# Kernel tuning notes

Hardware: AMD Instinct MI355X
Metric: run time of the kernel (lower is better)

## Reference

```python
import jax, jax.numpy as jnp
import numpy as np

B, N, DIM = 2, 2048, 1024
HEADS, DH = 16, 64
INNER = HEADS * DH
LN_EPS = 1e-5


def setup_inputs() -> dict:
    key = jax.random.key(0)
    ks = jax.random.split(key, 3)
    x = jax.random.normal(ks[0], (B, N, DIM), dtype=jnp.float32)
    ln_w = jnp.ones((DIM,), dtype=jnp.float32)
    ln_b = jnp.zeros((DIM,), dtype=jnp.float32)
    w_qkv = jax.random.normal(ks[1], (DIM, 3 * INNER), dtype=jnp.float32) * (DIM ** -0.5)
    w_out = jax.random.normal(ks[2], (INNER, DIM), dtype=jnp.float32) * (INNER ** -0.5)
    b_out = jnp.zeros((DIM,), dtype=jnp.float32)
    return {"x": x, "ln_w": ln_w, "ln_b": ln_b, "w_qkv": w_qkv, "w_out": w_out, "b_out": b_out}


def _rope(q, k):
    # q, k: (b, h, n, d) with d even; interleaved RoPE matching the torch module.
    n, d = q.shape[-2], q.shape[-1]
    inv_freq = jnp.exp(jnp.arange(0, d, 2, dtype=jnp.float32) * (-jnp.log(jnp.float32(10000.0)) / d))
    ang = jnp.arange(n, dtype=jnp.float32)[:, None] * inv_freq[None, :]  # (n, d/2)
    cos = jnp.repeat(jnp.cos(ang), 2, axis=-1)  # (n, d) -> broadcast over b,h
    sin = jnp.repeat(jnp.sin(ang), 2, axis=-1)

    def rot(t):
        t2 = t.reshape(*t.shape[:-1], d // 2, 2)  # pairs (even, odd)
        t2 = jnp.stack([-t2[..., 1], t2[..., 0]], axis=-1).reshape(t.shape)
        return t * cos + t2 * sin

    return rot(q), rot(k)


def reference(x, ln_w, ln_b, w_qkv, w_out, b_out):
    # LayerNorm
    mu = jnp.mean(x, axis=-1, keepdims=True)
    var = jnp.var(x, axis=-1, keepdims=True)
    xn = (x - mu) * jax.lax.rsqrt(var + LN_EPS) * ln_w + ln_b
    # QKV projection (no bias)
    qkv = xn @ w_qkv  # (b, n, 3*inner)
    q, k, v = jnp.split(qkv, 3, axis=-1)
    split_heads = lambda t: t.reshape(B, N, HEADS, DH).transpose(0, 2, 1, 3)  # b h n d
    q, k, v = split_heads(q), split_heads(k), split_heads(v)
    q, k = _rope(q, k)
    scale = DH ** -0.5
    dots = jnp.einsum('bhid,bhjd->bhij', q, k) * scale
    attn = jax.nn.softmax(dots, axis=-1)
    out = jnp.einsum('bhij,bhjd->bhid', attn, v)
    out = out.transpose(0, 2, 1, 3).reshape(B, N, INNER)  # b n (h d)
    return out @ w_out + b_out
```

## Files before the change

### kernel.cpp

```cpp
#include <hip/hip_runtime.h>

typedef unsigned short u16;
typedef unsigned int   u32;
typedef __bf16 bf16x8 __attribute__((ext_vector_type(8)));
typedef __bf16 bf16x2 __attribute__((ext_vector_type(2)));
typedef float  f32x4  __attribute__((ext_vector_type(4)));

#define B_     2
#define N_     2048
#define DIM_   1024
#define HEADS_ 16
#define DH_    64
#define BH_    (B_*HEADS_)
#define ROWS_  (B_*N_)

__device__ __forceinline__ u16 f2b(float f) {
  union { __bf16 h; u16 u; } v; v.h = (__bf16)f; return v.u;
}
__device__ __forceinline__ u32 pkb(float a, float b) {
  bf16x2 t; t[0] = (__bf16)a; t[1] = (__bf16)b;
  union { bf16x2 v; u32 u; } c; c.v = t; return c.u;
}
__device__ __forceinline__ float b2f(u16 h) {
  union { u32 u; float f; } v; v.u = ((u32)h) << 16;
  return v.f;
}
__device__ __forceinline__ void gload16(const void* g, void* l) {
  __builtin_amdgcn_global_load_lds(
      (const __attribute__((address_space(1))) void*)g,
      (__attribute__((address_space(3))) void*)l, 16, 0, 0);
}
__device__ __forceinline__ f32x4 mfma16(bf16x8 a, bf16x8 b, f32x4 c) {
  return __builtin_amdgcn_mfma_f32_16x16x32_bf16(a, b, c, 0, 0, 0);
}

__global__ __launch_bounds__(256) void prep_kernel(
    const float* __restrict__ x, const float* __restrict__ lw,
    const float* __restrict__ lb, const float* __restrict__ wqkv,
    const float* __restrict__ wout, u16* __restrict__ xn,
    u16* __restrict__ wqt, u16* __restrict__ wot) {
  __shared__ float tile[32][33];
  int blk = blockIdx.x, t = threadIdx.x;
  if (blk < 4096) {
    int r = blk;
    const float4* xr = (const float4*)(x + (size_t)r * DIM_);
    float4 v = xr[t];
    float s  = v.x + v.y + v.z + v.w;
    float s2 = v.x*v.x + v.y*v.y + v.z*v.z + v.w*v.w;
    #pragma unroll
    for (int off = 32; off >= 1; off >>= 1) {
      s  += __shfl_down(s, off);
      s2 += __shfl_down(s2, off);
    }
    int w = t >> 6, lane = t & 63;
    if (lane == 0) { tile[0][w] = s; tile[1][w] = s2; }
    __syncthreads();
    if (t == 0) {
      float S = tile[0][0]+tile[0][1]+tile[0][2]+tile[0][3];
      float S2 = tile[1][0]+tile[1][1]+tile[1][2]+tile[1][3];
      float mu = S * (1.0f/DIM_);
      float var = S2 * (1.0f/DIM_) - mu*mu;
      tile[2][0] = mu; tile[2][1] = rsqrtf(var + 1e-5f);
    }
    __syncthreads();
    float mu = tile[2][0], rs = tile[2][1];
    float4 wv = ((const float4*)lw)[t];
    float4 bv = ((const float4*)lb)[t];
    u32 lo = pkb((v.x-mu)*rs*wv.x + bv.x, (v.y-mu)*rs*wv.y + bv.y);
    u32 hi = pkb((v.z-mu)*rs*wv.z + bv.z, (v.w-mu)*rs*wv.w + bv.w);
    ((uint2*)xn)[(size_t)r*256 + t] = make_uint2(lo, hi);
  } else {
    const float* in; u16* outp; int R, C, c0, r0;
    if (blk < 7168) {
      int b2 = blk - 4096;
      in = wqkv; outp = wqt; R = 1024; C = 3072;
      c0 = (b2 % 96) * 32; r0 = (b2 / 96) * 32;
    } else {
      int b2 = blk - 7168;
      in = wout; outp = wot; R = 1024; C = 1024;
      c0 = (b2 & 31) * 32; r0 = (b2 >> 5) * 32;
    }
    int tx = t & 31, ty = t >> 5;
    #pragma unroll
    for (int i = 0; i < 4; i++)
      tile[ty + i*8][tx] = in[(size_t)(r0 + ty + i*8) * C + c0 + tx];
    __syncthreads();
    #pragma unroll
    for (int i = 0; i < 4; i++)
      outp[(size_t)(c0 + ty + i*8) * R + r0 + tx] = f2b(tile[tx][ty + i*8]);
  }
}

__global__ __launch_bounds__(256) void gemm_qkv(
    const u16* __restrict__ A, const u16* __restrict__ Bt,
    u16* __restrict__ qo, u16* __restrict__ ko, u16* __restrict__ vo) {
  const int K = 1024;
  __shared__ __align__(16) u16 lA[128*32];
  __shared__ __align__(16) u16 lB[128*32];
  int tid = threadIdx.x;
  int lane = tid & 63;
  int w = tid >> 6, wm = w >> 1, wn = w & 1;
  int l15 = lane & 15, g = lane >> 4;
  int bm = blockIdx.x, bn = blockIdx.y;
  const f32x4 z = {0.f, 0.f, 0.f, 0.f};
  f32x4 acc[4][4];
  #pragma unroll
  for (int i = 0; i < 4; i++)
    #pragma unroll
    for (int j = 0; j < 4; j++)
      acc[i][j] = z;
  int sslot = (tid & 3) ^ ((tid >> 3) & 3);
  const u16* ag = A  + (size_t)(bm*128 + (tid>>2)) * K + sslot*8;
  const u16* bg = Bt + (size_t)(bn*128 + (tid>>2)) * K + sslot*8;
  u16* la = lA + tid*8;
  u16* lb = lB + tid*8;
  for (int k0 = 0; k0 < K; k0 += 32) {
    gload16(ag + k0,                la);
    gload16(ag + (size_t)64*K + k0, la + 2048);
    gload16(bg + k0,                lb);
    gload16(bg + (size_t)64*K + k0, lb + 2048);
    __syncthreads();
    bf16x8 af[4], bfr[4];
    #pragma unroll
    for (int mt = 0; mt < 4; mt++) {
      int R = wm*64 + mt*16 + l15;
      af[mt] = *(const bf16x8*)(lA + R*32 + (g ^ ((R >> 1) & 3))*8);
    }
    #pragma unroll
    for (int nt = 0; nt < 4; nt++) {
      int R = wn*64 + nt*16 + l15;
      bfr[nt] = *(const bf16x8*)(lB + R*32 + (g ^ ((R >> 1) & 3))*8);
    }
    __builtin_amdgcn_s_setprio(1);
    #pragma unroll
    for (int mt = 0; mt < 4; mt++)
      #pragma unroll
      for (int nt = 0; nt < 4; nt++)
        acc[mt][nt] = mfma16(af[mt], bfr[nt], acc[mt][nt]);
    __builtin_amdgcn_s_setprio(0);
    __syncthreads();
  }
  #pragma unroll
  for (int mt = 0; mt < 4; mt++) {
    #pragma unroll
    for (int nt = 0; nt < 4; nt++) {
      #pragma unroll
      for (int reg = 0; reg < 4; reg++) {
        int rr = bm*128 + wm*64 + mt*16 + g*4 + reg;
        int cc = bn*128 + wn*64 + nt*16 + l15;
        float val = acc[mt][nt][reg];
        int which = cc >> 10, inner = cc & 1023;
        int h = inner >> 6, dd = inner & 63;
        int b = rr >> 11, np = rr & 2047;
        int bh = b*HEADS_ + h;
        if (which == 0)      qo[((size_t)(bh*2048 + np))*64 + dd] = f2b(val);
        else if (which == 1) ko[((size_t)(bh*2048 + np))*64 + dd] = f2b(val);
        else                 vo[((size_t)(bh*64 + dd))*2048 + np] = f2b(val);
      }
    }
  }
}

__global__ __launch_bounds__(256) void rope_k_kernel(u16* k) {
  int tid = blockIdx.x * 256 + threadIdx.x;
  int row = tid >> 3, sub = tid & 7;
  int n = row & 2047;
  u32* kp = (u32*)(k + (size_t)row * 64 + sub * 8);
  uint4 uk = *(uint4*)kp;
  float c4[4], s4[4];
  #pragma unroll
  for (int j = 0; j < 4; j++) {
    int p = sub*4 + j;
    float freq = expf(-(2.0f * (float)p) * (9.210340371976184f / 64.0f));
    float ang = (float)n * freq;
    __sincosf(ang, &s4[j], &c4[j]);
  }
#define ROPE_K(u, c, s) { \
    float e = b2f((u16)(u)), o = b2f((u16)((u) >> 16)); \
    (u) = pkb(e*(c) - o*(s), o*(c) + e*(s)); }
  ROPE_K(uk.x, c4[0], s4[0]) ROPE_K(uk.y, c4[1], s4[1])
  ROPE_K(uk.z, c4[2], s4[2]) ROPE_K(uk.w, c4[3], s4[3])
#undef ROPE_K
  *(uint4*)kp = uk;
}

__global__ __launch_bounds__(256) void gemm_out(
    const u16* __restrict__ A, const u16* __restrict__ Bt,
    const float* __restrict__ bias, float* __restrict__ out) {
  const int K = 1024, N = 1024;
  __shared__ __align__(16) u16 lA[128*32];
  __shared__ __align__(16) u16 lB[64*32];
  int tid = threadIdx.x;
  int lane = tid & 63;
  int w = tid >> 6, wm = w >> 1, wn = w & 1;
  int l15 = lane & 15, g = lane >> 4;
  int bm = blockIdx.x, bn = blockIdx.y;
  const f32x4 z = {0.f, 0.f, 0.f, 0.f};
  f32x4 acc[4][2];
  #pragma unroll
  for (int i = 0; i < 4; i++)
    #pragma unroll
    for (int j = 0; j < 2; j++)
      acc[i][j] = z;
  int sslot = (tid & 3) ^ ((tid >> 3) & 3);
  const u16* ag = A  + (size_t)(bm*128 + (tid>>2)) * K + sslot*8;
  const u16* bg = Bt + (size_t)(bn*64 + (tid>>2)) * K + sslot*8;
  u16* la = lA + tid*8;
  u16* lb = lB + tid*8;
  for (int k0 = 0; k0 < K; k0 += 32) {
    gload16(ag + k0,                la);
    gload16(ag + (size_t)64*K + k0, la + 2048);
    gload16(bg + k0,                lb);
    __syncthreads();
    bf16x8 af[4], bfr[2];
    #pragma unroll
    for (int mt = 0; mt < 4; mt++) {
      int R = wm*64 + mt*16 + l15;
      af[mt] = *(const bf16x8*)(lA + R*32 + (g ^ ((R >> 1) & 3))*8);
    }
    #pragma unroll
    for (int nt = 0; nt < 2; nt++) {
      int R = wn*32 + nt*16 + l15;
      bfr[nt] = *(const bf16x8*)(lB + R*32 + (g ^ ((R >> 1) & 3))*8);
    }
    __builtin_amdgcn_s_setprio(1);
    #pragma unroll
    for (int mt = 0; mt < 4; mt++)
      #pragma unroll
      for (int nt = 0; nt < 2; nt++)
        acc[mt][nt] = mfma16(af[mt], bfr[nt], acc[mt][nt]);
    __builtin_amdgcn_s_setprio(0);
    __syncthreads();
  }
  #pragma unroll
  for (int mt = 0; mt < 4; mt++)
    #pragma unroll
    for (int nt = 0; nt < 2; nt++)
      #pragma unroll
      for (int reg = 0; reg < 4; reg++) {
        int rr = bm*128 + wm*64 + mt*16 + g*4 + reg;
        int cc = bn*64 + wn*32 + nt*16 + l15;
        out[(size_t)rr * N + cc] = acc[mt][nt][reg] + bias[cc];
      }
}

__global__ __launch_bounds__(512, 4) void flash_attn(
    const u16* __restrict__ qbf, const u16* __restrict__ kbf,
    const u16* __restrict__ vt, u16* __restrict__ aout) {
  __shared__ __align__(16) char smem[49152];
  int tid = threadIdx.x;
  int w = tid >> 6, lane = tid & 63;
  int l15 = lane & 15, g = lane >> 4;
  int p = w & 3, rho = w >> 2;
  int lin = blockIdx.x;
  int nb = (lin & 7) * 64 + (lin >> 3);
  int bh = nb >> 4, qb = nb & 15;
  const f32x4 z = {0.f, 0.f, 0.f, 0.f};
  const u16* qrow_base = qbf + ((size_t)bh*2048 + qb*128 + p*32) * 64;
  const float qs = 0.125f * 1.4426950408889634f;
  bf16x8 Qf[2][2];
  #pragma unroll
  for (int qt = 0; qt < 2; qt++) {
    int n = qb*128 + p*32 + qt*16 + l15;
    #pragma unroll
    for (int dh = 0; dh < 2; dh++) {
      union { bf16x8 v; u32 u[4]; } f;
      f.v = *(const bf16x8*)(qrow_base + (qt*16 + l15)*64 + dh*32 + g*8);
      #pragma unroll
      for (int j = 0; j < 4; j++) {
        int pidx = dh*16 + g*4 + j;
        float freq = expf(-(2.0f * (float)pidx) * (9.210340371976184f / 64.0f));
        float sn, cn;
        __sincosf((float)n * freq, &sn, &cn);
        float e = b2f((u16)f.u[j]), o = b2f((u16)(f.u[j] >> 16));
        f.u[j] = pkb((e*cn - o*sn)*qs, (o*cn + e*sn)*qs);
      }
      Qf[qt][dh] = f.v;
    }
  }
  const char* kb = (const char*)(kbf + (size_t)bh * 2048 * 64);
  const char* vb = (const char*)(vt  + (size_t)bh * 64 * 2048);
  int srow = tid >> 3;
  int soff = ((tid & 7) * 16) ^ ((srow & 7) << 4);
  int sl = srow & 31;
  int ksrc = (srow & 32) | (((sl >> 2) & 3) << 3) | (((sl >> 4) & 1) << 2) | (sl & 3);
  const int swz = (l15 & 7) << 4;

  const size_t kgo = (size_t)ksrc * 128 + soff;
  const size_t vgo = (size_t)srow * 4096 + soff;
  const int ldk = tid * 16;
  const int ldv = 24576 + tid * 16;
  int koff[2][2], voff[4];
  #pragma unroll
  for (int kt = 0; kt < 2; kt++)
    #pragma unroll
    for (int dh = 0; dh < 2; dh++)
      koff[kt][dh] = (rho*32 + kt*16 + l15)*128 + ((dh*64 + g*16) ^ swz);
  #pragma unroll
  for (int dt = 0; dt < 4; dt++)
    voff[dt] = 24576 + (dt*16 + l15)*128 + ((rho*64 + g*16) ^ swz);

  bf16x8 ones;
  #pragma unroll
  for (int i = 0; i < 8; i++) ones[i] = (__bf16)1.0f;

  f32x4 den[2] = {z, z};
  f32x4 o[4][2];
  #pragma unroll
  for (int i = 0; i < 4; i++)
    #pragma unroll
    for (int j = 0; j < 2; j++)
      o[i][j] = z;

#define STAGE(T, BUF) { \
    gload16(kb + (size_t)(T)*8192 + kgo, smem + (BUF)*8192 + ldk); \
    gload16(vb + (size_t)(T)*128  + vgo, smem + (BUF)*8192 + ldv); }

#define FBODY(T, CUR, PFB, DOSTAGE, WM) { \
    if (DOSTAGE) STAGE((T) + 2, PFB) \
    f32x4 st[2][2]; \
    bf16x8 ka[2][2]; \
    _Pragma("unroll") \
    for (int kt = 0; kt < 2; kt++) \
      _Pragma("unroll") \
      for (int dh = 0; dh < 2; dh++) \
        ka[kt][dh] = *(const bf16x8*)(smem + (CUR)*8192 + koff[kt][dh]); \
    __builtin_amdgcn_s_setprio(1); \
    _Pragma("unroll") \
    for (int kt = 0; kt < 2; kt++) \
      _Pragma("unroll") \
      for (int qt = 0; qt < 2; qt++) { \
        f32x4 a = mfma16(ka[kt][0], Qf[qt][0], z); \
        st[kt][qt] = mfma16(ka[kt][1], Qf[qt][1], a); \
      } \
    __builtin_amdgcn_s_setprio(0); \
    _Pragma("unroll") \
    for (int kt = 0; kt < 2; kt++) \
      _Pragma("unroll") \
      for (int qt = 0; qt < 2; qt++) \
        _Pragma("unroll") \
        for (int r = 0; r < 4; r++) \
          st[kt][qt][r] = __builtin_amdgcn_exp2f(st[kt][qt][r]); \
    bf16x8 vf[4]; \
    _Pragma("unroll") \
    for (int dt = 0; dt < 4; dt++) \
      vf[dt] = *(const bf16x8*)(smem + (CUR)*8192 + voff[dt]); \
    __builtin_amdgcn_s_setprio(1); \
    _Pragma("unroll") \
    for (int qt = 0; qt < 2; qt++) { \
      union { u32 u[4]; bf16x8 v; } pf; \
      pf.u[0] = pkb(st[0][qt][0], st[0][qt][1]); \
      pf.u[1] = pkb(st[0][qt][2], st[0][qt][3]); \
      pf.u[2] = pkb(st[1][qt][0], st[1][qt][1]); \
      pf.u[3] = pkb(st[1][qt][2], st[1][qt][3]); \
      den[qt] = mfma16(ones, pf.v, den[qt]); \
      _Pragma("unroll") \
      for (int dt = 0; dt < 4; dt++) \
        o[dt][qt] = mfma16(vf[dt], pf.v, o[dt][qt]); \
    } \
    __builtin_amdgcn_s_setprio(0); \
    if ((WM) == 2) { \
      asm volatile("s_waitcnt vmcnt(2)" ::: "memory"); \
      __builtin_amdgcn_s_barrier(); \
    } else if ((WM) == 0) { \
      asm volatile("s_waitcnt vmcnt(0)" ::: "memory"); \
      __builtin_amdgcn_s_barrier(); \
    } }

  STAGE(0, 0)
  STAGE(1, 1)
  asm volatile("s_waitcnt vmcnt(2)" ::: "memory");
  __builtin_amdgcn_s_barrier();

  #pragma unroll 1
  for (int tb = 0; tb < 30; tb += 3) {
    FBODY(tb + 0, 0, 2, 1, 2)
    FBODY(tb + 1, 1, 0, 1, 2)
    FBODY(tb + 2, 2, 1, 1, 2)
  }
  FBODY(30, 0, 0, 0, 0)
  FBODY(31, 1, 0, 0, 3)
#undef STAGE
#undef FBODY

  float ls[2] = {den[0][0], den[1][0]};
  __syncthreads();

  float* lspx = (float*)(smem + 32768);
  if (rho == 1) {
    #pragma unroll
    for (int dt = 0; dt < 4; dt++)
      #pragma unroll
      for (int qt = 0; qt < 2; qt++) {
        int ql = qt*16 + l15;
        int off = p*8192 + ql*256 + ((dt*64 + g*16) ^ ((ql & 7) << 4));
        *(f32x4*)(smem + off) = o[dt][qt];
      }
    if (g == 0) {
      lspx[p*64 + l15]      = ls[0];
      lspx[p*64 + 16 + l15] = ls[1];
    }
  }
  __syncthreads();
  float rls[2] = {0.f, 0.f};
  if (rho == 0) {
    #pragma unroll
    for (int qt = 0; qt < 2; qt++)
      rls[qt] = 1.0f / (ls[qt] + lspx[p*64 + qt*16 + l15]);
    #pragma unroll
    for (int dt = 0; dt < 4; dt++)
      #pragma unroll
      for (int qt = 0; qt < 2; qt++) {
        int ql = qt*16 + l15;
        int off = p*8192 + ql*256 + ((dt*64 + g*16) ^ ((ql & 7) << 4));
        o[dt][qt] += *(const f32x4*)(smem + off);
      }
  }
  __syncthreads();
  if (rho == 0) {
    #pragma unroll
    for (int dt = 0; dt < 4; dt++)
      #pragma unroll
      for (int qt = 0; qt < 2; qt++) {
        int ql = qt*16 + l15;
        u32 w0 = pkb(o[dt][qt][0]*rls[qt], o[dt][qt][1]*rls[qt]);
        u32 w1 = pkb(o[dt][qt][2]*rls[qt], o[dt][qt][3]*rls[qt]);
        int d2 = dt*32 + g*8;
        *(uint2*)(smem + p*8192 + ql*128 + (d2 ^ ((ql & 7) << 4))) =
            make_uint2(w0, w1);
      }
  }
  __syncthreads();
  int row = tid >> 2;
  int b = bh >> 4, h = bh & 15;
  int n = qb*128 + row;
  #pragma unroll
  for (int j = 0; j < 2; j++) {
    int slot = (tid & 3)*2 + j;
    uint4 rv = *(const uint4*)(smem + (row >> 5)*8192 + (row & 31)*128
                               + ((slot*16) ^ ((row & 7) << 4)));
    *(uint4*)(aout + ((size_t)(b*2048 + n))*1024 + h*64 + slot*8) = rv;
  }
}

extern "C" void kernel_launch(void* const* d_in, const int* in_sizes, int n_in,
                              void* d_out, int out_size, void* d_ws, size_t ws_size,
                              hipStream_t stream) {
  const float* x    = (const float*)d_in[0];
  const float* lw   = (const float*)d_in[1];
  const float* lb   = (const float*)d_in[2];
  const float* wqkv = (const float*)d_in[3];
  const float* wout = (const float*)d_in[4];
  const float* bout = (const float*)d_in[5];
  float* out = (float*)d_out;

  char* ws = (char*)d_ws;
  size_t off = 0;
  auto alloc = [&](size_t bytes) {
    char* p = ws + off;
    off += (bytes + 255) & ~(size_t)255;
    return p;
  };
  u16* xn   = (u16*)alloc((size_t)ROWS_*DIM_*2);
  u16* wqt  = (u16*)alloc((size_t)3072*1024*2);
  u16* wot  = (u16*)alloc((size_t)1024*1024*2);
  u16* qb   = (u16*)alloc((size_t)BH_*2048*64*2);
  u16* kb   = (u16*)alloc((size_t)BH_*2048*64*2);
  u16* vtb  = (u16*)alloc((size_t)BH_*2048*64*2);
  u16* aout = (u16*)alloc((size_t)ROWS_*1024*2);

  prep_kernel<<<8192, 256, 0, stream>>>(x, lw, lb, wqkv, wout, xn, wqt, wot);
  gemm_qkv<<<dim3(32, 24), 256, 0, stream>>>(xn, wqt, qb, kb, vtb);
  rope_k_kernel<<<2048, 256, 0, stream>>>(kb);
  flash_attn<<<512, 512, 0, stream>>>(qb, kb, vtb, aout);
  gemm_out<<<dim3(32, 16), 256, 0, stream>>>(aout, wot, bout, out);
}
```

Before: 110.6 us.

## Triple-buffer LDS in QKV GEMM with async prefetch two tiles ahead

```diff
diff --git a/kernel.cpp b/kernel.cpp
--- a/kernel.cpp
+++ b/kernel.cpp
@@ -95,8 +95,7 @@
     const u16* __restrict__ A, const u16* __restrict__ Bt,
     u16* __restrict__ qo, u16* __restrict__ ko, u16* __restrict__ vo) {
   const int K = 1024;
-  __shared__ __align__(16) u16 lA[128*32];
-  __shared__ __align__(16) u16 lB[128*32];
+  __shared__ __align__(16) char smem[49152];
   int tid = threadIdx.x;
   int lane = tid & 63;
   int w = tid >> 6, wm = w >> 1, wn = w & 1;
@@ -112,34 +111,65 @@
   int sslot = (tid & 3) ^ ((tid >> 3) & 3);
   const u16* ag = A  + (size_t)(bm*128 + (tid>>2)) * K + sslot*8;
   const u16* bg = Bt + (size_t)(bn*128 + (tid>>2)) * K + sslot*8;
-  u16* la = lA + tid*8;
-  u16* lb = lB + tid*8;
-  for (int k0 = 0; k0 < K; k0 += 32) {
-    gload16(ag + k0,                la);
-    gload16(ag + (size_t)64*K + k0, la + 2048);
-    gload16(bg + k0,                lb);
-    gload16(bg + (size_t)64*K + k0, lb + 2048);
-    __syncthreads();
-    bf16x8 af[4], bfr[4];
-    #pragma unroll
-    for (int mt = 0; mt < 4; mt++) {
-      int R = wm*64 + mt*16 + l15;
-      af[mt] = *(const bf16x8*)(lA + R*32 + (g ^ ((R >> 1) & 3))*8);
-    }
-    #pragma unroll
-    for (int nt = 0; nt < 4; nt++) {
-      int R = wn*64 + nt*16 + l15;
-      bfr[nt] = *(const bf16x8*)(lB + R*32 + (g ^ ((R >> 1) & 3))*8);
-    }
-    __builtin_amdgcn_s_setprio(1);
-    #pragma unroll
-    for (int mt = 0; mt < 4; mt++)
-      #pragma unroll
-      for (int nt = 0; nt < 4; nt++)
-        acc[mt][nt] = mfma16(af[mt], bfr[nt], acc[mt][nt]);
-    __builtin_amdgcn_s_setprio(0);
-    __syncthreads();
-  }
+  const int ldd = tid * 16;
+  int aoff[4], boff[4];
+  #pragma unroll
+  for (int mt = 0; mt < 4; mt++) {
+    int R = wm*64 + mt*16 + l15;
+    aoff[mt] = R*64 + (g ^ ((R >> 1) & 3))*16;
+  }
+  #pragma unroll
+  for (int nt = 0; nt < 4; nt++) {
+    int R = wn*64 + nt*16 + l15;
+    boff[nt] = 24576 + R*64 + (g ^ ((R >> 1) & 3))*16;
+  }
+
+#define GSTAGE(T, BUF) { \
+    gload16(ag + (T)*32,                smem + (BUF)*8192 + ldd); \
+    gload16(ag + (size_t)64*K + (T)*32, smem + (BUF)*8192 + 4096 + ldd); \
+    gload16(bg + (T)*32,                smem + 24576 + (BUF)*8192 + ldd); \
+    gload16(bg + (size_t)64*K + (T)*32, smem + 24576 + (BUF)*8192 + 4096 + ldd); }
+
+#define GBODY(T, CUR, PFB, DOSTAGE, WM) { \
+    if (DOSTAGE) GSTAGE((T) + 2, PFB) \
+    bf16x8 af[4], bfr[4]; \
+    _Pragma("unroll") \
+    for (int mt = 0; mt < 4; mt++) \
+      af[mt] = *(const bf16x8*)(smem + (CUR)*8192 + aoff[mt]); \
+    _Pragma("unroll") \
+    for (int nt = 0; nt < 4; nt++) \
+      bfr[nt] = *(const bf16x8*)(smem + (CUR)*8192 + boff[nt]); \
+    __builtin_amdgcn_s_setprio(1); \
+    _Pragma("unroll") \
+    for (int mt = 0; mt < 4; mt++) \
+      _Pragma("unroll") \
+      for (int nt = 0; nt < 4; nt++) \
+        acc[mt][nt] = mfma16(af[mt], bfr[nt], acc[mt][nt]); \
+    __builtin_amdgcn_s_setprio(0); \
+    if ((WM) == 4) { \
+      asm volatile("s_waitcnt vmcnt(4)" ::: "memory"); \
+      __builtin_amdgcn_s_barrier(); \
+    } else if ((WM) == 0) { \
+      asm volatile("s_waitcnt vmcnt(0)" ::: "memory"); \
+      __builtin_amdgcn_s_barrier(); \
+    } }
+
+  GSTAGE(0, 0)
+  GSTAGE(1, 1)
+  asm volatile("s_waitcnt vmcnt(4)" ::: "memory");
+  __builtin_amdgcn_s_barrier();
+
+  #pragma unroll 1
+  for (int tb = 0; tb < 30; tb += 3) {
+    GBODY(tb + 0, 0, 2, 1, 4)
+    GBODY(tb + 1, 1, 0, 1, 4)
+    GBODY(tb + 2, 2, 1, 1, 4)
+  }
+  GBODY(30, 0, 0, 0, 0)
+  GBODY(31, 1, 0, 0, 9)
+#undef GSTAGE
+#undef GBODY
+
   #pragma unroll
   for (int mt = 0; mt < 4; mt++) {
     #pragma unroll
```

Result: no change. 111.8 us (+1.1%).
